# Performance work log

Hardware: AMD Instinct MI355X
Metric: run time of the kernel (lower is better)

## Reference

```python
import math
import jax, jax.numpy as jnp
import numpy as np

NUM_COARSE = 8192
NUM_FINE = 16384
L_POINT = 10
L_DIR = 4
POINT_DIM = 60
DIR_DIM = 24
WIDTH = 256
DEPTH = 8
LAST = 1e-4


def _encode(x, L):
    # Original loops l over even ints 0,2,...,2L-2 with freq 2**l -> 2^(2k)*pi
    freqs = (2.0 ** (2.0 * jnp.arange(L, dtype=x.dtype))) * jnp.asarray(math.pi, x.dtype)
    ang = x[..., None] * freqs                                  # (..., 3, L)
    enc = jnp.stack([jnp.sin(ang), jnp.cos(ang)], axis=-1)      # (..., 3, L, 2)
    return enc.reshape(x.shape[:-1] + (3 * 2 * L,))


def _mlp(pt_enc, dir_enc, W0, b0, Wh, bh, Wsig, bsig, Wcol, bcol):
    h = jax.nn.relu(pt_enc @ W0 + b0)
    for i in range(DEPTH - 1):                                  # 7 hidden ReLU layers
        h = jax.nn.relu(h @ Wh[i] + bh[i])
    h = h @ Wh[DEPTH - 1] + bh[DEPTH - 1]                       # final linear, no activation
    sigma = jax.nn.sigmoid(h @ Wsig + bsig)                     # (N, 1)
    dirs = jnp.broadcast_to(dir_enc, (h.shape[0], DIR_DIM))
    color = jax.nn.sigmoid(jnp.concatenate([dirs, h], axis=1) @ Wcol + bcol)  # (N, 3)
    return color, sigma


def _net_out(t_array, d_cam, dir_enc, trans_mat, params):
    n = t_array.shape[0]
    # camera-space points: d_cam with z replaced by t
    pts_cam = jnp.concatenate([
        jnp.broadcast_to(d_cam[:2], (n, 2)),
        t_array[:, None],
        jnp.broadcast_to(d_cam[3:], (n, 1))], axis=1)           # (n, 4)
    pts_wrd = (pts_cam @ trans_mat.T)[:, :3]                    # (n, 3)
    return _mlp(_encode(pts_wrd, L_POINT), dir_enc, *params)


def _color_cum(delta, sigma, color):
    sd = delta * sigma
    T = jnp.exp(-jnp.cumsum(sd))
    w = T * (1.0 - jnp.exp(-sd))
    return jnp.sum(color * w[:, None], axis=0)                  # (3,)


def _render(hor, ver, trans_mat, near, far, params):
    one = jnp.ones_like(hor)
    d_cam = jnp.stack([hor, -ver, one, one])                    # render_ray gets -ver already applied by caller sign flip
    d_wrd = trans_mat @ d_cam
    dir_enc = _encode(d_wrd[:3], L_DIR)                         # (24,)
    t_coarse = jnp.linspace(near, far, NUM_COARSE)
    color_co, sigma_co = _net_out(t_coarse, d_cam, dir_enc, trans_mat, params)
    # inverse-CDF resampling (vectorized version of the per-sample loop)
    s = sigma_co[:, 0]
    cdf = jnp.cumsum(s)                                         # strictly increasing (sigmoid > 0)
    dt = t_coarse[1] - t_coarse[0]
    slope_inv = dt / s[1:]
    t_inv = jnp.linspace(cdf[0], cdf[-1], NUM_FINE + 2)[1:-1]
    idx = jnp.clip(jnp.searchsorted(cdf, t_inv, side='left') - 1, 0, NUM_COARSE - 2)
    t_fine = t_coarse[idx] + (t_inv - cdf[idx]) * slope_inv[idx]
    color_fi, sigma_fi = _net_out(t_fine, d_cam, dir_enc, trans_mat, params)
    # bundle sort: original sorts each row independently (torch.sort along dim=1)
    t_all = jnp.concatenate([t_coarse, t_fine])
    color_all = jnp.concatenate([color_co, color_fi])
    sigma_all = jnp.concatenate([sigma_co[:, 0], sigma_fi[:, 0]])
    bundle = jnp.sort(jnp.concatenate([t_all[None], color_all.T, sigma_all[None]], axis=0), axis=1)
    t = bundle[0]
    color = bundle[1:4].T
    sigma = bundle[4]
    delta = jnp.concatenate([t[1:] - t[:-1], jnp.full((1,), LAST, t.dtype)])
    delta_co = jnp.broadcast_to((far - near) / NUM_COARSE, (NUM_COARSE,))
    C_coarse = _color_cum(delta_co, sigma_co[:, 0], color_co)
    C_fine = _color_cum(delta, sigma, color)
    return C_coarse, C_fine


def setup_inputs():
    key = jax.random.key(0)
    ks = jax.random.split(key, 12)

    def dense(k, fi, fo):
        kw, kb = jax.random.split(k)
        W = jax.random.normal(kw, (fi, fo), jnp.float32) / jnp.sqrt(jnp.asarray(fi, jnp.float32))
        b = jax.random.normal(kb, (fo,), jnp.float32) * 0.01
        return W, b

    W0, b0 = dense(ks[0], POINT_DIM, WIDTH)
    Whb = [dense(ks[1 + i], WIDTH, WIDTH) for i in range(DEPTH)]
    Wh = jnp.stack([w for w, _ in Whb])
    bh = jnp.stack([b for _, b in Whb])
    Wsig, bsig = dense(ks[9], WIDTH, 1)
    Wcol, bcol = dense(ks[10], WIDTH + DIR_DIM, 3)
    trans_mat = jnp.eye(4, dtype=jnp.float32) + 0.1 * jax.random.normal(ks[11], (4, 4), jnp.float32)
    return {
        'hor': jnp.asarray(0.3, jnp.float32), 'ver': jnp.asarray(-0.2, jnp.float32),
        'trans_mat': trans_mat,
        'near': jnp.asarray(2.0, jnp.float32), 'far': jnp.asarray(6.0, jnp.float32),
        'W0': W0, 'b0': b0, 'Wh': Wh, 'bh': bh,
        'Wsig': Wsig, 'bsig': bsig, 'Wcol': Wcol, 'bcol': bcol,
    }


def reference(hor, ver, trans_mat, near, far, W0, b0, Wh, bh, Wsig, bsig, Wcol, bcol):
    params = (W0, b0, Wh, bh, Wsig, bsig, Wcol, bcol)
    # NeRFModel.forward negates ver before render_ray
    return _render(hor, -ver, trans_mat, near, far, params)
```

## Files before the change

kernel.cpp:

```cpp
#include <hip/hip_runtime.h>
#include <math.h>

#define NC 8192
#define NF 16384
#define NT 24576
#define RN 12288
#define LASTD 1e-4f
#define PI_F 3.14159265358979323846f

#define WS_CONST 0
#define WS_TFINE 64
#define WS_SIGCO (WS_TFINE + NF)
#define WS_COLCO (WS_SIGCO + NC)
#define WS_SIGFI (WS_COLCO + 3*NC)
#define WS_COLFI (WS_SIGFI + NF)
#define WS_SRT   (WS_COLFI + 3*NF)
#define WS_RAD   (WS_SRT + 5*NT)
#define WS_CDF   (WS_RAD + 4*NT)
#define WS_WT    (WS_CDF + NC)
#define WS_FP    (WS_WT + 135168)
#define WS_CP    (WS_FP + 32)

typedef __attribute__((ext_vector_type(4))) float f32x4;
typedef __attribute__((ext_vector_type(2))) long i64x2;

static __device__ inline unsigned char f2e4m3(float x){
  unsigned pk = (unsigned)__builtin_amdgcn_cvt_pk_fp8_f32(x, 0.f, 0, false);
  return (unsigned char)(pk & 0xff);
}
static __device__ inline float e4m3f(unsigned char b){
  return __builtin_amdgcn_cvt_f32_fp8((int)b, 0);
}

__global__ __launch_bounds__(256) void k_prep_w(
    const float* __restrict__ W0, const float* __restrict__ Wh,
    unsigned char* __restrict__ Wt,
    const float* hor_, const float* ver_, const float* tm,
    const float* near_, const float* far_,
    const float* Wcol, const float* bcol, float* cst)
{
  if (blockIdx.x == 528) {
    if (threadIdx.x != 0) return;
    float hor = hor_[0], ver = ver_[0], nearv = near_[0], farv = far_[0];
    float dw[3];
    for (int j = 0; j < 3; ++j)
      dw[j] = tm[j*4+0]*hor + tm[j*4+1]*ver + tm[j*4+2] + tm[j*4+3];
    float enc[24];
    for (int i = 0; i < 3; ++i)
      for (int l = 0; l < 4; ++l) {
        float f = PI_F * exp2f(2.f*(float)l);
        float ang = dw[i]*f;
        enc[i*8 + l*2]     = sinf(ang);
        enc[i*8 + l*2 + 1] = cosf(ang);
      }
    for (int c = 0; c < 3; ++c) {
      float s = bcol[c];
      for (int d = 0; d < 24; ++d) s += enc[d]*Wcol[d*3+c];
      cst[6+c] = s;
    }
    for (int j = 0; j < 3; ++j) {
      cst[0+j] = tm[j*4+0]*hor + tm[j*4+1]*ver + tm[j*4+3];
      cst[3+j] = tm[j*4+2];
    }
    cst[9]  = nearv;
    cst[10] = (farv - nearv) / (float)(NC - 1);
    cst[11] = (farv - nearv) / (float)NC;
    return;
  }
  int base = (blockIdx.x*256 + threadIdx.x)*4;
  for (int e = base; e < base+4; ++e) {
    int c = e >> 13;
    if (c >= 66) break;
    int r = e & 8191;
    int w_ = r >> 10;
    int q = r & 1023;
    int ln = q >> 4;
    int rest = q & 15;
    int mt = rest >> 3, j = rest & 7;
    int out = (w_*2 + mt)*16 + (ln & 15);
    int kk = (ln >> 4)*8 + j;
    float v;
    if (c < 2) {
      int k = c*32 + kk;
      v = (k < 60) ? W0[k*256 + out] : 0.f;
    } else {
      int m = (c-2) >> 3, kc = (c-2) & 7;
      v = Wh[m*65536 + (kc*32+kk)*256 + out];
    }
    Wt[e] = f2e4m3(v);
  }
}

template<int NTL>
__global__ __launch_bounds__(512, 1) void k_mlp_mfma(
    const float* __restrict__ cst, const unsigned char* __restrict__ Wt,
    const float* __restrict__ b0, const float* __restrict__ bh,
    const float* __restrict__ Wsig, const float* __restrict__ bsig,
    const float* __restrict__ Wcol,
    const float* __restrict__ tf, int npts,
    float* __restrict__ sig_out, float* __restrict__ col_out)
{
  __shared__ __align__(16) unsigned char hbuf[NTL*16*256];
  __shared__ __align__(16) float bbuf[9*256];
  const int tid = threadIdx.x;
  const int w = tid >> 6, lane = tid & 63;
  const int lo = lane & 15, hi = lane >> 4;
  const int p0 = blockIdx.x * (NTL*16);

  if (tid < NTL*16*3) {
    int p = tid / 3, i = tid - p*3;
    int gp = p0 + p;
    float step = cst[10], nearv = cst[9];
    float t = tf ? tf[gp] : fmaf(step, (float)gp, nearv);
    float x = fmaf(cst[3+i], t, cst[0+i]);
    float s, c;
    sincosf(PI_F * x, &s, &c);
    unsigned char* row = &hbuf[p*256];
    #pragma unroll
    for (int l = 0; l < 10; ++l) {
      int d0 = i*20 + l*2;
      row[((((d0  )>>3) ^ (p&7))<<3) + ((d0  )&7)] = f2e4m3(s);
      row[((((d0+1)>>3) ^ (p&7))<<3) + ((d0+1)&7)] = f2e4m3(c);
      float s2 = 2.f*s*c, c2 = (c-s)*(c+s);
      s = 2.f*s2*c2; c = (c2-s2)*(c2+s2);
    }
    if (i == 0) {
      #pragma unroll
      for (int d = 60; d < 64; ++d)
        row[(((d>>3) ^ (p&7))<<3) + (d&7)] = 0;
    }
  }
  for (int i = tid; i < 9*256; i += 512) {
    int j = i >> 8, t = i & 255;
    bbuf[i] = (j == 0) ? b0[t] : bh[(j-1)*256 + t];
  }
  __syncthreads();

  unsigned boff[NTL];
  #pragma unroll
  for (int ni = 0; ni < NTL; ++ni) {
    int pp = ni*16 + lo;
    boff[ni] = (unsigned)(pp*256 + ((hi ^ (pp&7))<<3));
  }
  const unsigned voff = (unsigned)(w*1024 + lane*16);
  i64x2 S0,S1,S2,S3,S4,S5,S6,S7;
  f32x4 acc[2][NTL];

#define GLD1(ra,cc) do{ \
  const unsigned char* s_ = Wt + ((size_t)(cc))*8192; \
  asm volatile("global_load_dwordx4 %0, %1, %2" \
    : "=&v"(ra) : "v"(voff), "s"(s_)); }while(0)

#define VMWQ(Q) do{ int nfc__ = 65-(Q); nfc__ = nfc__>7?7:nfc__; \
  switch(nfc__){ \
    case 7: asm volatile("s_waitcnt vmcnt(7)":::"memory"); break; \
    case 6: asm volatile("s_waitcnt vmcnt(6)":::"memory"); break; \
    case 5: asm volatile("s_waitcnt vmcnt(5)":::"memory"); break; \
    case 4: asm volatile("s_waitcnt vmcnt(4)":::"memory"); break; \
    case 3: asm volatile("s_waitcnt vmcnt(3)":::"memory"); break; \
    case 2: asm volatile("s_waitcnt vmcnt(2)":::"memory"); break; \
    case 1: asm volatile("s_waitcnt vmcnt(1)":::"memory"); break; \
    default: asm volatile("s_waitcnt vmcnt(0)":::"memory"); break; } \
  __builtin_amdgcn_sched_barrier(0); }while(0)

#define STEP(ra,KK,Q) do{ \
  long bfr_[NTL]; \
  _Pragma("unroll") \
  for(int ni=0;ni<NTL;++ni) \
    bfr_[ni] = *(const long*)((const char*)hbuf + (boff[ni] ^ ((unsigned)(KK)<<5))); \
  VMWQ(Q); \
  _Pragma("unroll") \
  for(int ni=0;ni<NTL;++ni){ \
    acc[0][ni]=__builtin_amdgcn_mfma_f32_16x16x32_fp8_fp8(ra[0],bfr_[ni],acc[0][ni],0,0,0); \
    acc[1][ni]=__builtin_amdgcn_mfma_f32_16x16x32_fp8_fp8(ra[1],bfr_[ni],acc[1][ni],0,0,0); } \
  __builtin_amdgcn_sched_barrier(0); \
  if ((Q)+8 <= 65) GLD1(ra,(Q)+8); \
}while(0)

  auto zacc = [&]() {
    const f32x4 z4 = {0.f,0.f,0.f,0.f};
    #pragma unroll
    for (int mi=0;mi<2;++mi)
      #pragma unroll
      for (int ni=0;ni<NTL;++ni) acc[mi][ni] = z4;
  };
  auto epilogue = [&](int l, bool relu) {
    const float* bias = &bbuf[l*256];
    #pragma unroll
    for (int mi=0;mi<2;++mi) {
      int mt = w*2+mi;
      f32x4 bv = *(const f32x4*)&bias[mt*16 + hi*4];
      #pragma unroll
      for (int ni=0;ni<NTL;++ni) {
        f32x4 v = acc[mi][ni];
        float o0=v[0]+bv[0], o1=v[1]+bv[1], o2=v[2]+bv[2], o3=v[3]+bv[3];
        if (relu){o0=fmaxf(o0,0.f);o1=fmaxf(o1,0.f);o2=fmaxf(o2,0.f);o3=fmaxf(o3,0.f);}
        unsigned pk = (unsigned)__builtin_amdgcn_cvt_pk_fp8_f32(o0, o1, 0, false);
        pk = (unsigned)__builtin_amdgcn_cvt_pk_fp8_f32(o2, o3, (int)pk, true);
        int pp = ni*16 + lo;
        int colu = mt*16 + hi*4;
        int sl = colu >> 3, off = colu & 7;
        *(unsigned*)((char*)hbuf + pp*256 + ((sl^(pp&7))<<3) + off) = pk;
      }
    }
  };

  GLD1(S0,0); GLD1(S1,1); GLD1(S2,2); GLD1(S3,3);
  GLD1(S4,4); GLD1(S5,5); GLD1(S6,6); GLD1(S7,7);

  zacc();
  STEP(S0, 0, 0);
  STEP(S1, 1, 1);
  __builtin_amdgcn_s_barrier();
  epilogue(0, true);
  asm volatile("s_waitcnt lgkmcnt(0)":::"memory");
  __builtin_amdgcn_sched_barrier(0);
  __builtin_amdgcn_s_barrier();

  #pragma unroll 1
  for (int l = 1; l < 9; ++l) {
    zacc();
    const int cb = 2 + (l-1)*8;
    STEP(S2, 0, cb+0);
    STEP(S3, 1, cb+1);
    STEP(S4, 2, cb+2);
    STEP(S5, 3, cb+3);
    STEP(S6, 4, cb+4);
    STEP(S7, 5, cb+5);
    STEP(S0, 6, cb+6);
    STEP(S1, 7, cb+7);
    __builtin_amdgcn_s_barrier();
    epilogue(l, l < 8);
    asm volatile("s_waitcnt lgkmcnt(0)":::"memory");
    __builtin_amdgcn_sched_barrier(0);
    __builtin_amdgcn_s_barrier();
  }
#undef GLD1
#undef VMWQ
#undef STEP

  if (tid < NTL*64) {
    int p = tid >> 2, s = tid & 3;
    float as_=0.f, a0=0.f, a1=0.f, a2=0.f;
    for (int q=0;q<8;++q) {
      int slot = s*8+q;
      const unsigned char* hb = &hbuf[p*256 + ((slot^(p&7))<<3)];
      #pragma unroll
      for (int j=0;j<8;++j) {
        float hf = e4m3f(hb[j]);
        int k = s*64 + q*8 + j;
        as_ = fmaf(hf, Wsig[k], as_);
        const float* wc = Wcol + 72 + k*3;
        a0 = fmaf(hf, wc[0], a0);
        a1 = fmaf(hf, wc[1], a1);
        a2 = fmaf(hf, wc[2], a2);
      }
    }
    as_ += __shfl_xor(as_,1); as_ += __shfl_xor(as_,2);
    a0 += __shfl_xor(a0,1); a0 += __shfl_xor(a0,2);
    a1 += __shfl_xor(a1,1); a1 += __shfl_xor(a1,2);
    a2 += __shfl_xor(a2,1); a2 += __shfl_xor(a2,2);
    if (s == 0) {
      sig_out[p0+p] = 1.f/(1.f+expf(-(as_ + bsig[0])));
      col_out[0*npts + p0+p] = 1.f/(1.f+expf(-(a0 + cst[6])));
      col_out[1*npts + p0+p] = 1.f/(1.f+expf(-(a1 + cst[7])));
      col_out[2*npts + p0+p] = 1.f/(1.f+expf(-(a2 + cst[8])));
    }
  }
}

__global__ __launch_bounds__(1024) void k_postco(
    const float* __restrict__ sigco, const float* __restrict__ colco,
    const float* __restrict__ cst, float* __restrict__ cdfg, float* __restrict__ outv)
{
  __shared__ float wsum[16];
  __shared__ float r0[16], r1[16], r2[16];
  const int tid = threadIdx.x;
  const int lane = tid & 63, wid = tid >> 6;
  float v[8], inc[8];
  float run = 0.f;
  #pragma unroll
  for (int j = 0; j < 8; ++j) { v[j] = sigco[tid*8+j]; run += v[j]; inc[j] = run; }
  float sc = run;
  #pragma unroll
  for (int off = 1; off < 64; off <<= 1) {
    float t = __shfl_up(sc, off);
    if (lane >= off) sc += t;
  }
  if (lane == 63) wsum[wid] = sc;
  __syncthreads();
  if (tid < 16) {
    float wv = wsum[tid];
    float s2 = wv;
    #pragma unroll
    for (int off = 1; off < 16; off <<= 1) {
      float t = __shfl_up(s2, off);
      if (tid >= off) s2 += t;
    }
    wsum[tid] = s2 - wv;
  }
  __syncthreads();
  float excl = wsum[wid] + (sc - run);
  float cv[8];
  #pragma unroll
  for (int j = 0; j < 8; ++j) cv[j] = excl + inc[j];
  *(f32x4*)&cdfg[tid*8]     = *(f32x4*)&cv[0];
  *(f32x4*)&cdfg[tid*8 + 4] = *(f32x4*)&cv[4];

  float dco = cst[11];
  float a0=0.f, a1=0.f, a2=0.f;
  #pragma unroll
  for (int j = 0; j < 8; ++j) {
    int i = tid*8+j;
    float T = expf(-dco*cv[j]);
    float w = T*(1.f-expf(-dco*v[j]));
    a0 += colco[i]*w; a1 += colco[NC+i]*w; a2 += colco[2*NC+i]*w;
  }
  for (int off = 32; off; off >>= 1) {
    a0 += __shfl_down(a0, off); a1 += __shfl_down(a1, off); a2 += __shfl_down(a2, off);
  }
  if (lane==0) { r0[wid]=a0; r1[wid]=a1; r2[wid]=a2; }
  __syncthreads();
  if (tid==0) {
    float s0=0,s1=0,s2=0;
    for (int i=0;i<16;++i){s0+=r0[i];s1+=r1[i];s2+=r2[i];}
    outv[0]=s0; outv[1]=s1; outv[2]=s2;
  }
}

__global__ __launch_bounds__(1024) void k_invcdf(
    const float* __restrict__ cdfg, const float* __restrict__ sigco,
    const float* __restrict__ cst, float* __restrict__ tfine)
{
  int j = blockIdx.x*1024 + threadIdx.x;
  float cdf0 = cdfg[0], cdfN = cdfg[NC-1];
  float stepi = (cdfN - cdf0) / (float)(NF+1);
  float nearv = cst[9], dt = cst[10];
  float tv = cdf0 + (float)(j+1)*stepi;
  int lo = 0, hi = NC;
  while (lo < hi) { int mid = (lo+hi)>>1; if (cdfg[mid] < tv) lo = mid+1; else hi = mid; }
  int idx = lo-1; idx = idx < 0 ? 0 : (idx > NC-2 ? NC-2 : idx);
  float sig1 = sigco[idx+1];
  tfine[j] = fmaf(dt, (float)idx, nearv) + (tv - cdfg[idx]) * (dt / sig1);
}

__global__ __launch_bounds__(1024) void k_radix(
    const float* __restrict__ sigco, const float* __restrict__ colco,
    const float* __restrict__ sigfi, const float* __restrict__ colfi,
    float* __restrict__ rad)
{
  __shared__ unsigned int buf[RN];
  __shared__ unsigned int wh[16][256];
  __shared__ unsigned int tot[256];
  __shared__ unsigned int dbase[256];
  const int tid = threadIdx.x;
  const int w = tid >> 6, lane = tid & 63;
  const int a = blockIdx.x >> 1, hf = blockIdx.x & 1;
  const unsigned long long below = (1ull << lane) - 1ull;

  unsigned int key[12];
  #pragma unroll
  for (int j = 0; j < 12; ++j) {
    int i = w*768 + j*64 + lane;
    int g = hf*RN + i;
    float v;
    if (a < 3) v = (g < NC) ? colco[a*NC+g] : colfi[a*NF + (g-NC)];
    else       v = (g < NC) ? sigco[g] : sigfi[g-NC];
    key[j] = __float_as_uint(v);
  }

  for (int p = 0; p < 4; ++p) {
    const int sh = p*8;
    for (int i = tid; i < 16*256; i += 1024) ((unsigned int*)wh)[i] = 0;
    __syncthreads();
    unsigned int lrk[12];
    #pragma unroll
    for (int j = 0; j < 12; ++j) {
      unsigned int d = (key[j] >> sh) & 255u;
      unsigned long long m = ~0ull;
      #pragma unroll
      for (int b = 0; b < 8; ++b) {
        unsigned long long bb = __ballot((d >> b) & 1u);
        m &= ((d >> b) & 1u) ? bb : ~bb;
      }
      unsigned int rkl = (unsigned int)__popcll(m & below);
      unsigned int base = wh[w][d];
      if (rkl == 0) wh[w][d] = base + (unsigned int)__popcll(m);
      lrk[j] = base + rkl;
    }
    __syncthreads();
    if (tid < 256) {
      unsigned int run2 = 0;
      #pragma unroll
      for (int ww = 0; ww < 16; ++ww) { unsigned int c = wh[ww][tid]; wh[ww][tid] = run2; run2 += c; }
      tot[tid] = run2;
    }
    __syncthreads();
    if (tid < 64) {
      unsigned int t0=tot[tid*4], t1=tot[tid*4+1], t2=tot[tid*4+2], t3=tot[tid*4+3];
      unsigned int ssum = t0+t1+t2+t3;
      unsigned int sc = ssum;
      for (int off=1; off<64; off<<=1) { unsigned int vv = __shfl_up((int)sc, off); if (lane>=off) sc += vv; }
      unsigned int ex = sc - ssum;
      dbase[tid*4] = ex; dbase[tid*4+1] = ex+t0; dbase[tid*4+2] = ex+t0+t1; dbase[tid*4+3] = ex+t0+t1+t2;
    }
    __syncthreads();
    #pragma unroll
    for (int j = 0; j < 12; ++j) {
      unsigned int d = (key[j] >> sh) & 255u;
      buf[dbase[d] + wh[w][d] + lrk[j]] = key[j];
    }
    __syncthreads();
    if (p < 3) {
      #pragma unroll
      for (int j = 0; j < 12; ++j) key[j] = buf[w*768 + j*64 + lane];
      __syncthreads();
    }
  }
  for (int i = tid; i < RN; i += 1024)
    rad[a*NT + hf*RN + i] = __uint_as_float(buf[i]);
}

__global__ __launch_bounds__(1024) void k_merge(
    const float* __restrict__ rad, const float* __restrict__ tfine,
    const float* __restrict__ cst, float* __restrict__ srt)
{
  const int row = blockIdx.x >> 2, q = blockIdx.x & 3;
  const float dt = cst[10], nv = cst[9];
  const bool isT = (row == 0);
  const float* A = isT ? (const float*)nullptr : rad + (row-1)*NT;
  const float* B = isT ? tfine : (A + RN);
  const int nA = isT ? NC : RN, nB = isT ? NF : RN;
  int k0 = q*6144 + (int)threadIdx.x*6;
  int lo = k0-nB; if (lo < 0) lo = 0;
  int hi = k0 < nA ? k0 : nA;
  while (lo < hi) {
    int mid = (lo+hi)>>1;
    float av = isT ? fmaf(dt,(float)mid,nv) : A[mid];
    if (av <= B[k0-mid-1]) lo = mid+1; else hi = mid;
  }
  int i = lo, j = k0 - lo;
  float* o = srt + row*NT;
  #pragma unroll
  for (int c = 0; c < 6; ++c) {
    float av = (i < nA) ? (isT ? fmaf(dt,(float)i,nv) : A[i]) : 0.f;
    bool ta = (j >= nB) || (i < nA && av <= B[j]);
    float v = ta ? av : B[j];
    if (ta) ++i; else ++j;
    o[k0+c] = v;
  }
}

__global__ __launch_bounds__(1024) void k_fpart(
    const float* __restrict__ srt, float* __restrict__ fpart)
{
  const float* trow = srt;
  const float* sgr = srt + 4*NT;
  __shared__ float wsum[16];
  int i = blockIdx.x*1024 + threadIdx.x;
  const int lane = threadIdx.x & 63, wid = threadIdx.x >> 6;
  float tcur = trow[i];
  float tnext = (i < NT-1) ? trow[i+1] : 0.f;
  float delta = (i == NT-1) ? LASTD : (tnext - tcur);
  float sd = delta * sgr[i];
  float s = sd;
  #pragma unroll
  for (int off = 32; off; off >>= 1) s += __shfl_down(s, off);
  if (lane == 0) wsum[wid] = s;
  __syncthreads();
  if (threadIdx.x == 0) {
    float t = 0.f;
    for (int k = 0; k < 16; ++k) t += wsum[k];
    fpart[blockIdx.x] = t;
  }
}

__global__ __launch_bounds__(1024) void k_fcomb(
    const float* __restrict__ srt, const float* __restrict__ fpart,
    float* __restrict__ cpart)
{
  const float* trow = srt;
  const float* c0r = srt + NT;
  const float* c1r = srt + 2*NT;
  const float* c2r = srt + 3*NT;
  const float* sgr = srt + 4*NT;
  __shared__ float wsum[16];
  __shared__ float r0[16], r1[16], r2[16];
  const int tid = threadIdx.x;
  const int lane = tid & 63, wid = tid >> 6;
  int i = blockIdx.x*1024 + tid;
  float off0 = 0.f;
  for (int k = 0; k < 24; ++k) off0 += (k < (int)blockIdx.x) ? fpart[k] : 0.f;

  float tcur = trow[i];
  float tnext = (i < NT-1) ? trow[i+1] : 0.f;
  float delta = (i == NT-1) ? LASTD : (tnext - tcur);
  float sd = delta * sgr[i];
  float sc = sd;
  #pragma unroll
  for (int off = 1; off < 64; off <<= 1) {
    float t = __shfl_up(sc, off);
    if (lane >= off) sc += t;
  }
  if (lane == 63) wsum[wid] = sc;
  __syncthreads();
  if (tid < 16) {
    float wv = wsum[tid];
    float s2 = wv;
    #pragma unroll
    for (int off = 1; off < 16; off <<= 1) {
      float t = __shfl_up(s2, off);
      if (tid >= off) s2 += t;
    }
    wsum[tid] = s2 - wv;
  }
  __syncthreads();
  float Sinc = off0 + wsum[wid] + sc;
  float T = expf(-Sinc);
  float w = T*(1.f-expf(-sd));
  float a0 = c0r[i]*w, a1 = c1r[i]*w, a2 = c2r[i]*w;
  #pragma unroll
  for (int off = 32; off; off >>= 1) {
    a0 += __shfl_down(a0, off); a1 += __shfl_down(a1, off); a2 += __shfl_down(a2, off);
  }
  if (lane==0) { r0[wid]=a0; r1[wid]=a1; r2[wid]=a2; }
  __syncthreads();
  if (tid==0) {
    float s0=0,s1=0,s2=0;
    for (int k=0;k<16;++k){s0+=r0[k];s1+=r1[k];s2+=r2[k];}
    cpart[blockIdx.x*3+0]=s0; cpart[blockIdx.x*3+1]=s1; cpart[blockIdx.x*3+2]=s2;
  }
}

__global__ void k_fsum(const float* __restrict__ cpart, float* __restrict__ outv)
{
  int c = threadIdx.x;
  if (c < 3) {
    float s = 0.f;
    for (int b = 0; b < 24; ++b) s += cpart[b*3 + c];
    outv[3 + c] = s;
  }
}

extern "C" void kernel_launch(void* const* d_in, const int* in_sizes, int n_in,
                              void* d_out, int out_size, void* d_ws, size_t ws_size,
                              hipStream_t stream) {
  (void)in_sizes; (void)n_in; (void)out_size; (void)ws_size;
  const float* hor  = (const float*)d_in[0];
  const float* ver  = (const float*)d_in[1];
  const float* tm   = (const float*)d_in[2];
  const float* nearp= (const float*)d_in[3];
  const float* farp = (const float*)d_in[4];
  const float* W0   = (const float*)d_in[5];
  const float* b0   = (const float*)d_in[6];
  const float* Wh   = (const float*)d_in[7];
  const float* bh   = (const float*)d_in[8];
  const float* Wsig = (const float*)d_in[9];
  const float* bsig = (const float*)d_in[10];
  const float* Wcol = (const float*)d_in[11];
  const float* bcol = (const float*)d_in[12];
  float* out = (float*)d_out;
  float* ws  = (float*)d_ws;

  float* cst   = ws + WS_CONST;
  float* tfine = ws + WS_TFINE;
  float* sigco = ws + WS_SIGCO;
  float* colco = ws + WS_COLCO;
  float* sigfi = ws + WS_SIGFI;
  float* colfi = ws + WS_COLFI;
  float* srt   = ws + WS_SRT;
  float* rad   = ws + WS_RAD;
  float* cdfg  = ws + WS_CDF;
  float* fpart = ws + WS_FP;
  float* cpart = ws + WS_CP;
  unsigned char* Wt = (unsigned char*)(ws + WS_WT);

  k_prep_w<<<dim3(529), dim3(256), 0, stream>>>(W0, Wh, Wt, hor, ver, tm, nearp, farp,
                                                Wcol, bcol, cst);
  k_mlp_mfma<2><<<dim3(NC/32), dim3(512), 0, stream>>>(cst, Wt, b0, bh, Wsig, bsig, Wcol,
                                                       (const float*)nullptr, NC, sigco, colco);
  k_postco<<<dim3(1), dim3(1024), 0, stream>>>(sigco, colco, cst, cdfg, out);
  k_invcdf<<<dim3(16), dim3(1024), 0, stream>>>(cdfg, sigco, cst, tfine);
  k_mlp_mfma<2><<<dim3(NF/32), dim3(512), 0, stream>>>(cst, Wt, b0, bh, Wsig, bsig, Wcol,
                                                       (const float*)tfine, NF, sigfi, colfi);
  k_radix<<<dim3(8), dim3(1024), 0, stream>>>(sigco, colco, sigfi, colfi, rad);
  k_merge<<<dim3(20), dim3(1024), 0, stream>>>(rad, tfine, cst, srt);
  k_fpart<<<dim3(24), dim3(1024), 0, stream>>>(srt, fpart);
  k_fcomb<<<dim3(24), dim3(1024), 0, stream>>>(srt, fpart, cpart);
  k_fsum<<<dim3(1), dim3(64), 0, stream>>>(cpart, out);
}
```

Before: 113.5 us.

## Split radix sort into quarter-sized blocks plus merge, and parallelize coarse color sum

The radix sort now runs on 16 blocks, each sorting a quarter-chunk of 6144 keys, and a new merge pass combines pairs of quarters into halves before the existing merge. The coarse post-processing is split into a single-block scan plus an 8-block color accumulation whose partial sums are reduced in k_fsum. The inverse-CDF kernel stages the CDF in shared memory for its binary search. The goal is to spread serial single-block and 8-block work across more CUs. The cost is two extra kernel launches and an extra global pass over the sorted data.

Result: faster. 104.1 us (-8.3%).

```diff
diff --git a/kernel.cpp b/kernel.cpp
--- a/kernel.cpp
+++ b/kernel.cpp
@@ -5,6 +5,7 @@
 #define NF 16384
 #define NT 24576
 #define RN 12288
+#define QN 6144
 #define LASTD 1e-4f
 #define PI_F 3.14159265358979323846f
 
@@ -20,6 +21,8 @@
 #define WS_WT    (WS_CDF + NC)
 #define WS_FP    (WS_WT + 135168)
 #define WS_CP    (WS_FP + 32)
+#define WS_CP2   (WS_CP + 128)
+#define WS_RAD4  (WS_CP2 + 32)
 
 typedef __attribute__((ext_vector_type(4))) float f32x4;
 typedef __attribute__((ext_vector_type(2))) long i64x2;
@@ -269,12 +272,10 @@
   }
 }
 
-__global__ __launch_bounds__(1024) void k_postco(
-    const float* __restrict__ sigco, const float* __restrict__ colco,
-    const float* __restrict__ cst, float* __restrict__ cdfg, float* __restrict__ outv)
+__global__ __launch_bounds__(1024) void k_scan1(
+    const float* __restrict__ sigco, float* __restrict__ cdfg)
 {
   __shared__ float wsum[16];
-  __shared__ float r0[16], r1[16], r2[16];
   const int tid = threadIdx.x;
   const int lane = tid & 63, wid = tid >> 6;
   float v[8], inc[8];
@@ -306,16 +307,22 @@
   for (int j = 0; j < 8; ++j) cv[j] = excl + inc[j];
   *(f32x4*)&cdfg[tid*8]     = *(f32x4*)&cv[0];
   *(f32x4*)&cdfg[tid*8 + 4] = *(f32x4*)&cv[4];
-
+}
+
+__global__ __launch_bounds__(1024) void k_ccoarse(
+    const float* __restrict__ sigco, const float* __restrict__ colco,
+    const float* __restrict__ cst, const float* __restrict__ cdfg,
+    float* __restrict__ cpart2)
+{
+  __shared__ float r0[16], r1[16], r2[16];
+  const int tid = threadIdx.x;
+  const int lane = tid & 63, wid = tid >> 6;
+  int i = blockIdx.x*1024 + tid;
   float dco = cst[11];
-  float a0=0.f, a1=0.f, a2=0.f;
-  #pragma unroll
-  for (int j = 0; j < 8; ++j) {
-    int i = tid*8+j;
-    float T = expf(-dco*cv[j]);
-    float w = T*(1.f-expf(-dco*v[j]));
-    a0 += colco[i]*w; a1 += colco[NC+i]*w; a2 += colco[2*NC+i]*w;
-  }
+  float T = expf(-dco*cdfg[i]);
+  float w = T*(1.f-expf(-dco*sigco[i]));
+  float a0 = colco[i]*w, a1 = colco[NC+i]*w, a2 = colco[2*NC+i]*w;
+  #pragma unroll
   for (int off = 32; off; off >>= 1) {
     a0 += __shfl_down(a0, off); a1 += __shfl_down(a1, off); a2 += __shfl_down(a2, off);
   }
@@ -323,8 +330,8 @@
   __syncthreads();
   if (tid==0) {
     float s0=0,s1=0,s2=0;
-    for (int i=0;i<16;++i){s0+=r0[i];s1+=r1[i];s2+=r2[i];}
-    outv[0]=s0; outv[1]=s1; outv[2]=s2;
+    for (int k=0;k<16;++k){s0+=r0[k];s1+=r1[k];s2+=r2[k];}
+    cpart2[blockIdx.x*3+0]=s0; cpart2[blockIdx.x*3+1]=s1; cpart2[blockIdx.x*3+2]=s2;
   }
 }
 
@@ -332,37 +339,42 @@
     const float* __restrict__ cdfg, const float* __restrict__ sigco,
     const float* __restrict__ cst, float* __restrict__ tfine)
 {
-  int j = blockIdx.x*1024 + threadIdx.x;
-  float cdf0 = cdfg[0], cdfN = cdfg[NC-1];
+  __shared__ float cdf[NC];
+  const int tid = threadIdx.x;
+  #pragma unroll
+  for (int r = 0; r < 8; ++r) cdf[r*1024 + tid] = cdfg[r*1024 + tid];
+  __syncthreads();
+  int j = blockIdx.x*1024 + tid;
+  float cdf0 = cdf[0], cdfN = cdf[NC-1];
   float stepi = (cdfN - cdf0) / (float)(NF+1);
   float nearv = cst[9], dt = cst[10];
   float tv = cdf0 + (float)(j+1)*stepi;
   int lo = 0, hi = NC;
-  while (lo < hi) { int mid = (lo+hi)>>1; if (cdfg[mid] < tv) lo = mid+1; else hi = mid; }
+  while (lo < hi) { int mid = (lo+hi)>>1; if (cdf[mid] < tv) lo = mid+1; else hi = mid; }
   int idx = lo-1; idx = idx < 0 ? 0 : (idx > NC-2 ? NC-2 : idx);
   float sig1 = sigco[idx+1];
-  tfine[j] = fmaf(dt, (float)idx, nearv) + (tv - cdfg[idx]) * (dt / sig1);
-}
-
-__global__ __launch_bounds__(1024) void k_radix(
+  tfine[j] = fmaf(dt, (float)idx, nearv) + (tv - cdf[idx]) * (dt / sig1);
+}
+
+__global__ __launch_bounds__(1024) void k_radix4(
     const float* __restrict__ sigco, const float* __restrict__ colco,
     const float* __restrict__ sigfi, const float* __restrict__ colfi,
-    float* __restrict__ rad)
-{
-  __shared__ unsigned int buf[RN];
+    float* __restrict__ rad4)
+{
+  __shared__ unsigned int buf[QN];
   __shared__ unsigned int wh[16][256];
   __shared__ unsigned int tot[256];
   __shared__ unsigned int dbase[256];
   const int tid = threadIdx.x;
   const int w = tid >> 6, lane = tid & 63;
-  const int a = blockIdx.x >> 1, hf = blockIdx.x & 1;
+  const int a = blockIdx.x >> 2, qq = blockIdx.x & 3;
   const unsigned long long below = (1ull << lane) - 1ull;
 
-  unsigned int key[12];
-  #pragma unroll
-  for (int j = 0; j < 12; ++j) {
-    int i = w*768 + j*64 + lane;
-    int g = hf*RN + i;
+  unsigned int key[6];
+  #pragma unroll
+  for (int j = 0; j < 6; ++j) {
+    int i = w*384 + j*64 + lane;
+    int g = qq*QN + i;
     float v;
     if (a < 3) v = (g < NC) ? colco[a*NC+g] : colfi[a*NF + (g-NC)];
     else       v = (g < NC) ? sigco[g] : sigfi[g-NC];
@@ -373,9 +385,9 @@
     const int sh = p*8;
     for (int i = tid; i < 16*256; i += 1024) ((unsigned int*)wh)[i] = 0;
     __syncthreads();
-    unsigned int lrk[12];
+    unsigned int lrk[6];
     #pragma unroll
-    for (int j = 0; j < 12; ++j) {
+    for (int j = 0; j < 6; ++j) {
       unsigned int d = (key[j] >> sh) & 255u;
       unsigned long long m = ~0ull;
       #pragma unroll
@@ -406,19 +418,44 @@
     }
     __syncthreads();
     #pragma unroll
-    for (int j = 0; j < 12; ++j) {
+    for (int j = 0; j < 6; ++j) {
       unsigned int d = (key[j] >> sh) & 255u;
       buf[dbase[d] + wh[w][d] + lrk[j]] = key[j];
     }
     __syncthreads();
     if (p < 3) {
       #pragma unroll
-      for (int j = 0; j < 12; ++j) key[j] = buf[w*768 + j*64 + lane];
+      for (int j = 0; j < 6; ++j) key[j] = buf[w*384 + j*64 + lane];
       __syncthreads();
     }
   }
-  for (int i = tid; i < RN; i += 1024)
-    rad[a*NT + hf*RN + i] = __uint_as_float(buf[i]);
+  for (int i = tid; i < QN; i += 1024)
+    rad4[a*NT + qq*QN + i] = __uint_as_float(buf[i]);
+}
+
+__global__ __launch_bounds__(1024) void k_merge2(
+    const float* __restrict__ rad4, float* __restrict__ rad)
+{
+  const int a = blockIdx.x >> 2, h = (blockIdx.x >> 1) & 1, s = blockIdx.x & 1;
+  const float* A = rad4 + a*NT + (2*h)*QN;
+  const float* B = A + QN;
+  float* o = rad + a*NT + h*RN;
+  int k0 = s*QN + (int)threadIdx.x*6;
+  int lo = k0-QN; if (lo < 0) lo = 0;
+  int hi = k0 < QN ? k0 : QN;
+  while (lo < hi) {
+    int mid = (lo+hi)>>1;
+    if (A[mid] <= B[k0-mid-1]) lo = mid+1; else hi = mid;
+  }
+  int i = lo, j = k0 - lo;
+  #pragma unroll
+  for (int c = 0; c < 6; ++c) {
+    float av = (i < QN) ? A[i] : 0.f;
+    bool ta = (j >= QN) || (i < QN && av <= B[j]);
+    float v = ta ? av : B[j];
+    if (ta) ++i; else ++j;
+    o[k0+c] = v;
+  }
 }
 
 __global__ __launch_bounds__(1024) void k_merge(
@@ -532,10 +569,14 @@
   }
 }
 
-__global__ void k_fsum(const float* __restrict__ cpart, float* __restrict__ outv)
+__global__ void k_fsum(const float* __restrict__ cpart, const float* __restrict__ cpart2,
+                       float* __restrict__ outv)
 {
   int c = threadIdx.x;
   if (c < 3) {
+    float s2 = 0.f;
+    for (int b = 0; b < 8; ++b) s2 += cpart2[b*3 + c];
+    outv[c] = s2;
     float s = 0.f;
     for (int b = 0; b < 24; ++b) s += cpart[b*3 + c];
     outv[3 + c] = s;
@@ -573,19 +614,23 @@
   float* cdfg  = ws + WS_CDF;
   float* fpart = ws + WS_FP;
   float* cpart = ws + WS_CP;
+  float* cpart2= ws + WS_CP2;
+  float* rad4  = ws + WS_RAD4;
   unsigned char* Wt = (unsigned char*)(ws + WS_WT);
 
   k_prep_w<<<dim3(529), dim3(256), 0, stream>>>(W0, Wh, Wt, hor, ver, tm, nearp, farp,
                                                 Wcol, bcol, cst);
   k_mlp_mfma<2><<<dim3(NC/32), dim3(512), 0, stream>>>(cst, Wt, b0, bh, Wsig, bsig, Wcol,
                                                        (const float*)nullptr, NC, sigco, colco);
-  k_postco<<<dim3(1), dim3(1024), 0, stream>>>(sigco, colco, cst, cdfg, out);
+  k_scan1<<<dim3(1), dim3(1024), 0, stream>>>(sigco, cdfg);
+  k_ccoarse<<<dim3(8), dim3(1024), 0, stream>>>(sigco, colco, cst, cdfg, cpart2);
   k_invcdf<<<dim3(16), dim3(1024), 0, stream>>>(cdfg, sigco, cst, tfine);
   k_mlp_mfma<2><<<dim3(NF/32), dim3(512), 0, stream>>>(cst, Wt, b0, bh, Wsig, bsig, Wcol,
                                                        (const float*)tfine, NF, sigfi, colfi);
-  k_radix<<<dim3(8), dim3(1024), 0, stream>>>(sigco, colco, sigfi, colfi, rad);
+  k_radix4<<<dim3(16), dim3(1024), 0, stream>>>(sigco, colco, sigfi, colfi, rad4);
+  k_merge2<<<dim3(16), dim3(1024), 0, stream>>>(rad4, rad);
   k_merge<<<dim3(20), dim3(1024), 0, stream>>>(rad, tfine, cst, srt);
   k_fpart<<<dim3(24), dim3(1024), 0, stream>>>(srt, fpart);
   k_fcomb<<<dim3(24), dim3(1024), 0, stream>>>(srt, fpart, cpart);
-  k_fsum<<<dim3(1), dim3(64), 0, stream>>>(cpart, out);
-}
+  k_fsum<<<dim3(1), dim3(64), 0, stream>>>(cpart, cpart2, out);
+}
```
